# Performance work log

Measured on AMD Instinct MI355X. Metric: run time of the kernel, lower is better.

Reference implementation:

```python
import jax, jax.numpy as jnp
import numpy as np

MARGIN = 1.9
SQUARED = False


def _pairwise_distances(e, squared):
    # e: [n, d]
    dot = e @ e.T                      # [n, n]
    sq = jnp.diagonal(dot)             # [n]
    d = jax.nn.relu(sq[None, :] - 2.0 * dot + sq[:, None])
    if not squared:
        zero_mask = (d == 0.0).astype(d.dtype)
        d = jnp.sqrt(d + zero_mask * 1e-16) * (1.0 - zero_mask)
    return d


def setup_inputs() -> dict:
    key = jax.random.key(0)
    k1, k2 = jax.random.split(key)
    embeddings = jax.random.normal(k1, (8, 80, 128), dtype=jnp.float32)
    labels = jax.random.randint(k2, (8, 80), 0, 10, dtype=jnp.int64)
    return {"embeddings": embeddings, "labels": labels}


def reference(embeddings, labels):
    b, s, dim = embeddings.shape
    e = embeddings.reshape(-1, dim)          # [n, d]
    lab = labels.reshape(-1)                 # [n]
    n = e.shape[0]

    dist = _pairwise_distances(e, SQUARED)   # [n, n]

    labels_equal = lab[None, :] == lab[:, None]
    not_diag = ~jnp.eye(n, dtype=bool)
    positive_mask = labels_equal & not_diag  # [n, n]
    negative_mask = ~labels_equal            # [n, n]

    # triplet tensor [anchor i, positive j, negative k]
    triplet = dist[:, :, None] - dist[:, None, :] + MARGIN  # [n, n, n]
    valid = positive_mask[:, :, None] & negative_mask[:, None, :]
    non_easy = valid & (triplet > 0)

    num_valid = valid.sum().astype(jnp.float32)
    num_non_easy = non_easy.sum().astype(jnp.float32)

    total = jnp.sum(triplet * non_easy.astype(triplet.dtype))
    loss = jnp.where(num_non_easy > 0, total / jnp.maximum(num_non_easy, 1.0), 0.0)
    frac = num_non_easy / (num_valid + 1e-16)
    return loss, num_valid, num_non_easy, frac
```

## Files before the change

### kernel.cpp

```cpp
#include <hip/hip_runtime.h>
#include <math.h>

#define MARGIN 1.9f
#define TILE 32
#define NMAX 1024

__global__ __launch_bounds__(256) void dist_kernel(
        const float* __restrict__ e, int n, int d,
        float* __restrict__ dist,
        unsigned int* __restrict__ done_counter)
{
    __shared__ float As[TILE * 132];
    __shared__ float Bs[TILE * 132];
    const int tid  = threadIdx.x;
    const int row0 = blockIdx.y * TILE;
    const int col0 = blockIdx.x * TILE;
    const int nf4  = d >> 2;

    if (blockIdx.x == 0 && blockIdx.y == 0 && tid == 0)
        *done_counter = 0u;

    const float4* eg  = (const float4*)e;
    float4* As4 = (float4*)As;
    float4* Bs4 = (float4*)Bs;
    for (int f = tid; f < TILE * nf4; f += 256) {
        int r = f / nf4, c = f - r * nf4;
        int ga = row0 + r; if (ga >= n) ga = n - 1;
        int gb = col0 + r; if (gb >= n) gb = n - 1;
        As4[r * 33 + c] = eg[(size_t)ga * nf4 + c];
        Bs4[r * 33 + c] = eg[(size_t)gb * nf4 + c];
    }
    __syncthreads();

    const int tx = tid & 15, ty = tid >> 4;
    float a00 = 0.f, a01 = 0.f, a10 = 0.f, a11 = 0.f;
    for (int t = 0; t < nf4; ++t) {
        float4 A0 = As4[ty * 33 + t];
        float4 A1 = As4[(ty + 16) * 33 + t];
        float4 B0 = Bs4[tx * 33 + t];
        float4 B1 = Bs4[(tx + 16) * 33 + t];
        float dx;
#define ACC(acc, A, B, comp) dx = A.comp - B.comp; acc = fmaf(dx, dx, acc)
        ACC(a00, A0, B0, x); ACC(a00, A0, B0, y); ACC(a00, A0, B0, z); ACC(a00, A0, B0, w);
        ACC(a01, A0, B1, x); ACC(a01, A0, B1, y); ACC(a01, A0, B1, z); ACC(a01, A0, B1, w);
        ACC(a10, A1, B0, x); ACC(a10, A1, B0, y); ACC(a10, A1, B0, z); ACC(a10, A1, B0, w);
        ACC(a11, A1, B1, x); ACC(a11, A1, B1, y); ACC(a11, A1, B1, z); ACC(a11, A1, B1, w);
#undef ACC
    }

    const int r0 = row0 + ty, r1 = row0 + ty + 16;
    const int c0 = col0 + tx, c1 = col0 + tx + 16;
#define EMIT(rr, cc, acc) if ((rr) < n && (cc) < n) \
        dist[(size_t)(rr) * n + (cc)] = ((acc) == 0.f) ? 0.f : sqrtf(acc)
    EMIT(r0, c0, a00); EMIT(r0, c1, a01);
    EMIT(r1, c0, a10); EMIT(r1, c1, a11);
#undef EMIT
}

__global__ __launch_bounds__(256) void triplet_kernel(
        const float* __restrict__ dist, const int* __restrict__ lab, int n,
        float* __restrict__ part_sum,
        unsigned int* __restrict__ part_ne,
        unsigned int* __restrict__ part_valid,
        unsigned int* __restrict__ done_counter,
        float* __restrict__ out)
{
    __shared__ float row[NMAX];
    __shared__ float pos[NMAX];
    __shared__ int   labs[NMAX];
    __shared__ int p_cnt, n_cnt;
    __shared__ float red_s[4];
    __shared__ unsigned int red_c[4];
    __shared__ unsigned int ticket_s;

    const int i    = blockIdx.x;
    const int tid  = threadIdx.x;
    const int lane = tid & 63;
    const int wv   = tid >> 6;

    if (tid == 0) { p_cnt = 0; n_cnt = 0; }
    for (int j = tid; j < n; j += 256) {
        row[j]  = dist[(size_t)i * n + j];
        labs[j] = lab[j];
    }
    __syncthreads();

    const int my_lab = labs[i];
    int local_neg = 0;
    for (int j = tid; j < n; j += 256) {
        if (labs[j] == my_lab) {
            if (j != i) { int k = atomicAdd(&p_cnt, 1); pos[k] = row[j]; }
        } else {
            local_neg++;
        }
    }
    for (int off = 32; off > 0; off >>= 1) local_neg += __shfl_down(local_neg, off, 64);
    if (lane == 0) atomicAdd(&n_cnt, local_neg);

    const float INF = __builtin_huge_valf();
    int j0 = tid, j1 = tid + 256, j2 = tid + 512, j3 = tid + 768;
    float n0 = (j0 < n && labs[j0] != my_lab) ? row[j0] : INF;
    float n1 = (j1 < n && labs[j1] != my_lab) ? row[j1] : INF;
    float n2 = (j2 < n && labs[j2] != my_lab) ? row[j2] : INF;
    float n3 = (j3 < n && labs[j3] != my_lab) ? row[j3] : INF;
    __syncthreads();
    const int P = p_cnt, N = n_cnt;

    float sum = 0.f;
    unsigned int c = 0;
    for (int j = 0; j < P; ++j) {
        float a = pos[j] + MARGIN;
        float t0 = a - n0; if (t0 > 0.f) { sum += t0; c++; }
        float t1 = a - n1; if (t1 > 0.f) { sum += t1; c++; }
        float t2 = a - n2; if (t2 > 0.f) { sum += t2; c++; }
        float t3 = a - n3; if (t3 > 0.f) { sum += t3; c++; }
    }

    for (int off = 32; off > 0; off >>= 1) {
        sum += __shfl_down(sum, off, 64);
        c   += __shfl_down(c,   off, 64);
    }
    if (lane == 0) { red_s[wv] = sum; red_c[wv] = c; }
    __syncthreads();

    if (tid == 0) {
        float s = 0.f; unsigned int cc = 0;
        for (int w = 0; w < 4; ++w) { s += red_s[w]; cc += red_c[w]; }
        part_sum[i]   = s;
        part_ne[i]    = cc;
        part_valid[i] = (unsigned int)P * (unsigned int)N;
        __threadfence();
        ticket_s = atomicAdd(done_counter, 1u);
    }
    __syncthreads();

    if (ticket_s == (unsigned int)gridDim.x - 1u) {
        __threadfence();
        volatile const float*        vs = (volatile const float*)part_sum;
        volatile const unsigned int* vn = (volatile const unsigned int*)part_ne;
        volatile const unsigned int* vv = (volatile const unsigned int*)part_valid;

        float s = 0.f;
        unsigned long long ne = 0, nv = 0;
        for (int b = tid; b < n; b += 256) {
            s  += vs[b];
            ne += vn[b];
            nv += vv[b];
        }
        for (int off = 32; off > 0; off >>= 1) {
            s  += __shfl_down(s,  off, 64);
            ne += __shfl_down(ne, off, 64);
            nv += __shfl_down(nv, off, 64);
        }
        __shared__ float fr_s[4];
        __shared__ unsigned long long fr_ne[4], fr_nv[4];
        if (lane == 0) { fr_s[wv] = s; fr_ne[wv] = ne; fr_nv[wv] = nv; }
        __syncthreads();
        if (tid == 0) {
            float ts = 0.f; unsigned long long tne = 0, tnv = 0;
            for (int w = 0; w < 4; ++w) { ts += fr_s[w]; tne += fr_ne[w]; tnv += fr_nv[w]; }
            float fne = (float)tne;
            float fnv = (float)tnv;
            out[0] = (fne > 0.f) ? (ts / fmaxf(fne, 1.f)) : 0.f;
            out[1] = fnv;
            out[2] = fne;
            out[3] = fne / (fnv + 1e-16f);
        }
    }
}

extern "C" void kernel_launch(void* const* d_in, const int* in_sizes, int n_in,
                              void* d_out, int out_size, void* d_ws, size_t ws_size,
                              hipStream_t stream) {
    const float* e  = (const float*)d_in[0];
    const int* lab  = (const int*)d_in[1];
    int n = in_sizes[1];
    int d = in_sizes[0] / n;

    char* ws = (char*)d_ws;
    float*        part_sum   = (float*)ws;
    unsigned int* part_ne    = (unsigned int*)(ws + (size_t)n * 4);
    unsigned int* part_valid = (unsigned int*)(ws + (size_t)n * 8);
    unsigned int* done_cnt   = (unsigned int*)(ws + (size_t)n * 12);
    size_t dist_off = ((size_t)n * 12 + 4 + 255) & ~(size_t)255;
    float*        dist       = (float*)(ws + dist_off);

    int nt = (n + TILE - 1) / TILE;
    dim3 grid(nt, nt);
    dist_kernel<<<grid, 256, 0, stream>>>(e, n, d, dist, done_cnt);
    triplet_kernel<<<n, 256, 0, stream>>>(dist, lab, n,
                                          part_sum, part_ne, part_valid,
                                          done_cnt, (float*)d_out);
}
```

Baseline: 82.88 us.

## Fuse distance and triplet kernels into one cooperative launch with grid sync

Merges the pairwise-distance kernel and the per-anchor triplet kernel into one cooperative kernel that uses a grid-wide sync between the phases, with the two-kernel path kept as a fallback if the cooperative launch fails. It reuses one shared-memory arena for both phases. The aim is to remove the second launch and the inter-kernel gap. In exchange it adds a grid barrier over 640 blocks, and cooperative launch may carry its own overhead or fail when the blocks cannot all be resident at once.

```diff
diff --git a/kernel.cpp b/kernel.cpp
--- a/kernel.cpp
+++ b/kernel.cpp
@@ -1,9 +1,177 @@
 #include <hip/hip_runtime.h>
+#include <hip/hip_cooperative_groups.h>
 #include <math.h>
+
+namespace cg = cooperative_groups;
 
 #define MARGIN 1.9f
 #define TILE 32
 #define NMAX 1024
+
+__global__ __launch_bounds__(256) void fused_all(
+        const float* __restrict__ e, const int* __restrict__ lab,
+        int n, int d,
+        float* __restrict__ dist,
+        float* __restrict__ part_sum,
+        unsigned int* __restrict__ part_ne,
+        unsigned int* __restrict__ part_valid,
+        unsigned int* __restrict__ done_counter,
+        float* __restrict__ out)
+{
+    __shared__ __align__(16) float arena[2 * TILE * 132];
+    __shared__ int p_cnt, n_cnt;
+    __shared__ float red_s[4];
+    __shared__ unsigned int red_c[4];
+    __shared__ unsigned int ticket_s;
+
+    const int tid  = threadIdx.x;
+    const int lane = tid & 63;
+    const int wv   = tid >> 6;
+    const int b    = blockIdx.x;
+    const int nf4  = d >> 2;
+    const int nt   = (n + TILE - 1) / TILE;
+    const float4* eg = (const float4*)e;
+
+    if (b == 0 && tid == 0) *done_counter = 0u;
+
+    if (b < nt * nt) {
+        float4* As4 = (float4*)arena;
+        float4* Bs4 = (float4*)(arena + TILE * 132);
+        const int row0 = (b / nt) * TILE;
+        const int col0 = (b % nt) * TILE;
+        for (int f = tid; f < TILE * nf4; f += 256) {
+            int r = f / nf4, c = f - r * nf4;
+            int ga = row0 + r; if (ga >= n) ga = n - 1;
+            int gb = col0 + r; if (gb >= n) gb = n - 1;
+            As4[r * 33 + c] = eg[(size_t)ga * nf4 + c];
+            Bs4[r * 33 + c] = eg[(size_t)gb * nf4 + c];
+        }
+        __syncthreads();
+
+        const int tx = tid & 15, ty = tid >> 4;
+        float a00 = 0.f, a01 = 0.f, a10 = 0.f, a11 = 0.f;
+        for (int t = 0; t < nf4; ++t) {
+            float4 A0 = As4[ty * 33 + t];
+            float4 A1 = As4[(ty + 16) * 33 + t];
+            float4 B0 = Bs4[tx * 33 + t];
+            float4 B1 = Bs4[tx * 33 + 16 * 33 + t];
+            float dx;
+#define ACC(acc, A, B, comp) dx = A.comp - B.comp; acc = fmaf(dx, dx, acc)
+            ACC(a00, A0, B0, x); ACC(a00, A0, B0, y); ACC(a00, A0, B0, z); ACC(a00, A0, B0, w);
+            ACC(a01, A0, B1, x); ACC(a01, A0, B1, y); ACC(a01, A0, B1, z); ACC(a01, A0, B1, w);
+            ACC(a10, A1, B0, x); ACC(a10, A1, B0, y); ACC(a10, A1, B0, z); ACC(a10, A1, B0, w);
+            ACC(a11, A1, B1, x); ACC(a11, A1, B1, y); ACC(a11, A1, B1, z); ACC(a11, A1, B1, w);
+#undef ACC
+        }
+
+        const int r0 = row0 + ty, r1 = row0 + ty + 16;
+        const int c0 = col0 + tx, c1 = col0 + tx + 16;
+#define EMIT(rr, cc, acc) if ((rr) < n && (cc) < n) \
+        dist[(size_t)(rr) * n + (cc)] = ((acc) == 0.f) ? 0.f : sqrtf(acc)
+        EMIT(r0, c0, a00); EMIT(r0, c1, a01);
+        EMIT(r1, c0, a10); EMIT(r1, c1, a11);
+#undef EMIT
+    }
+
+    cg::this_grid().sync();
+
+    const int i = b;
+    if (i < n) {
+        float* row  = arena;
+        float* pos  = arena + NMAX;
+        int*   labs = (int*)(arena + 2 * NMAX);
+
+        if (tid == 0) { p_cnt = 0; n_cnt = 0; }
+        for (int j = tid; j < n; j += 256) {
+            row[j]  = dist[(size_t)i * n + j];
+            labs[j] = lab[j];
+        }
+        __syncthreads();
+
+        const int my_lab = labs[i];
+        int local_neg = 0;
+        for (int j = tid; j < n; j += 256) {
+            if (labs[j] == my_lab) {
+                if (j != i) { int k = atomicAdd(&p_cnt, 1); pos[k] = row[j]; }
+            } else {
+                local_neg++;
+            }
+        }
+        for (int off = 32; off > 0; off >>= 1) local_neg += __shfl_down(local_neg, off, 64);
+        if (lane == 0) atomicAdd(&n_cnt, local_neg);
+
+        const float INF = __builtin_huge_valf();
+        int j0 = tid, j1 = tid + 256, j2 = tid + 512, j3 = tid + 768;
+        float n0 = (j0 < n && labs[j0] != my_lab) ? row[j0] : INF;
+        float n1 = (j1 < n && labs[j1] != my_lab) ? row[j1] : INF;
+        float n2 = (j2 < n && labs[j2] != my_lab) ? row[j2] : INF;
+        float n3 = (j3 < n && labs[j3] != my_lab) ? row[j3] : INF;
+        __syncthreads();
+        const int P = p_cnt, N = n_cnt;
+
+        float sum = 0.f;
+        unsigned int c = 0;
+        for (int j = 0; j < P; ++j) {
+            float a = pos[j] + MARGIN;
+            float t0 = a - n0; if (t0 > 0.f) { sum += t0; c++; }
+            float t1 = a - n1; if (t1 > 0.f) { sum += t1; c++; }
+            float t2 = a - n2; if (t2 > 0.f) { sum += t2; c++; }
+            float t3 = a - n3; if (t3 > 0.f) { sum += t3; c++; }
+        }
+
+        for (int off = 32; off > 0; off >>= 1) {
+            sum += __shfl_down(sum, off, 64);
+            c   += __shfl_down(c,   off, 64);
+        }
+        if (lane == 0) { red_s[wv] = sum; red_c[wv] = c; }
+        __syncthreads();
+
+        if (tid == 0) {
+            float s = 0.f; unsigned int cc = 0;
+            for (int w = 0; w < 4; ++w) { s += red_s[w]; cc += red_c[w]; }
+            part_sum[i]   = s;
+            part_ne[i]    = cc;
+            part_valid[i] = (unsigned int)P * (unsigned int)N;
+            __threadfence();
+            ticket_s = atomicAdd(done_counter, 1u);
+        }
+        __syncthreads();
+
+        if (ticket_s == (unsigned int)n - 1u) {
+            __threadfence();
+            volatile const float*        vs = (volatile const float*)part_sum;
+            volatile const unsigned int* vn = (volatile const unsigned int*)part_ne;
+            volatile const unsigned int* vv = (volatile const unsigned int*)part_valid;
+
+            float s = 0.f;
+            unsigned long long ne = 0, nv = 0;
+            for (int q = tid; q < n; q += 256) {
+                s  += vs[q];
+                ne += vn[q];
+                nv += vv[q];
+            }
+            for (int off = 32; off > 0; off >>= 1) {
+                s  += __shfl_down(s,  off, 64);
+                ne += __shfl_down(ne, off, 64);
+                nv += __shfl_down(nv, off, 64);
+            }
+            __shared__ float fr_s[4];
+            __shared__ unsigned long long fr_ne[4], fr_nv[4];
+            if (lane == 0) { fr_s[wv] = s; fr_ne[wv] = ne; fr_nv[wv] = nv; }
+            __syncthreads();
+            if (tid == 0) {
+                float ts = 0.f; unsigned long long tne = 0, tnv = 0;
+                for (int w = 0; w < 4; ++w) { ts += fr_s[w]; tne += fr_ne[w]; tnv += fr_nv[w]; }
+                float fne = (float)tne;
+                float fnv = (float)tnv;
+                out[0] = (fne > 0.f) ? (ts / fmaxf(fne, 1.f)) : 0.f;
+                out[1] = fnv;
+                out[2] = fne;
+                out[3] = fne / (fnv + 1e-16f);
+            }
+        }
+    }
+}
 
 __global__ __launch_bounds__(256) void dist_kernel(
         const float* __restrict__ e, int n, int d,
@@ -142,10 +310,10 @@
 
         float s = 0.f;
         unsigned long long ne = 0, nv = 0;
-        for (int b = tid; b < n; b += 256) {
-            s  += vs[b];
-            ne += vn[b];
-            nv += vv[b];
+        for (int q = tid; q < n; q += 256) {
+            s  += vs[q];
+            ne += vn[q];
+            nv += vv[q];
         }
         for (int off = 32; off > 0; off >>= 1) {
             s  += __shfl_down(s,  off, 64);
@@ -184,11 +352,22 @@
     unsigned int* done_cnt   = (unsigned int*)(ws + (size_t)n * 12);
     size_t dist_off = ((size_t)n * 12 + 4 + 255) & ~(size_t)255;
     float*        dist       = (float*)(ws + dist_off);
+    float*        outp       = (float*)d_out;
 
     int nt = (n + TILE - 1) / TILE;
-    dim3 grid(nt, nt);
-    dist_kernel<<<grid, 256, 0, stream>>>(e, n, d, dist, done_cnt);
-    triplet_kernel<<<n, 256, 0, stream>>>(dist, lab, n,
-                                          part_sum, part_ne, part_valid,
-                                          done_cnt, (float*)d_out);
+    int nblk = n > nt * nt ? n : nt * nt;
+
+    void* args[] = { (void*)&e, (void*)&lab, (void*)&n, (void*)&d, (void*)&dist,
+                     (void*)&part_sum, (void*)&part_ne, (void*)&part_valid,
+                     (void*)&done_cnt, (void*)&outp };
+    hipError_t err = hipLaunchCooperativeKernel((const void*)fused_all,
+                                                dim3(nblk), dim3(256),
+                                                args, 0, stream);
+    if (err != hipSuccess) {
+        dim3 grid(nt, nt);
+        dist_kernel<<<grid, 256, 0, stream>>>(e, n, d, dist, done_cnt);
+        triplet_kernel<<<n, 256, 0, stream>>>(dist, lab, n,
+                                              part_sum, part_ne, part_valid,
+                                              done_cnt, outp);
+    }
 }
```

After: 160.3 us. +93.4%, slower.
